# Kernel tuning notes

Measured on AMD Instinct MI355X. Metric: run time of the kernel, lower is better.

## Reference

```python
import jax, jax.numpy as jnp
import numpy as np

N = 50000          # num_nodes
E = 800000         # general (base) edge count
R_BASE = 3         # base relation types
R = 2 * R_BASE + 1 # base + inverse + self-loop relation
D_IN = 64
D_HID = 64
D_OUT = 64


def _glorot(k, shape):
    # xavier_uniform with relu gain, fan over last two dims
    gain = np.sqrt(2.0)
    bound = gain * np.sqrt(6.0 / (shape[-2] + shape[-1]))
    return jax.random.uniform(k, shape, jnp.float32, -bound, bound)


def setup_inputs() -> dict:
    key = jax.random.key(0)
    ks = jax.random.split(key, 6)
    x = jax.random.normal(ks[0], (N, D_IN), dtype=jnp.float32)
    src = jax.random.randint(ks[1], (E,), 0, N)
    dst = jax.random.randint(ks[2], (E,), 0, N)
    et = jax.random.randint(ks[3], (E,), 0, R_BASE)
    nodes = jnp.arange(N)
    # triples = [original edges, inverse edges (type+R_BASE), self-loops (type 2*R_BASE)]
    triples = jnp.concatenate([
        jnp.stack([src, et, dst], axis=1),
        jnp.stack([dst, et + R_BASE, src], axis=1),
        jnp.stack([nodes, jnp.full((N,), 2 * R_BASE), nodes], axis=1),
    ], axis=0).astype(jnp.int64)
    w1 = _glorot(ks[4], (R, D_IN, D_HID))
    w2 = _glorot(ks[5], (R, D_HID, D_OUT))
    b1 = jnp.zeros((D_HID,), jnp.float32)
    b2 = jnp.zeros((D_OUT,), jnp.float32)
    return {"x": x, "w1": w1, "b1": b1, "w2": w2, "b2": b2,
            "triples": triples, "num_nodes": N, "num_edge_types": R}


def _rgcn_layer(x, W, b, triples, num_nodes, num_rels):
    # vertical stacking: sparse adj [R*N, N], entry (r*N+src, dst) = 1, row-normalised
    src, et, dst = triples[:, 0], triples[:, 1], triples[:, 2]
    rows = et * num_nodes + src                     # [T] row index in stacked adj
    counts = jnp.zeros((num_rels * num_nodes,), x.dtype).at[rows].add(1.0)
    vals = 1.0 / counts[rows]                       # per-edge row-normalised weight
    msgs = vals[:, None] * x[dst]                   # [T, d] gathered + scaled messages
    af = jax.ops.segment_sum(msgs, rows, num_segments=num_rels * num_nodes)
    af = af.reshape(num_rels, num_nodes, x.shape[1])  # [R, N, d]
    return jnp.einsum('rio,rni->no', W, af) + b


def reference(x, w1, b1, w2, b2, triples, num_nodes, num_edge_types):
    h = _rgcn_layer(x, w1, b1, triples, num_nodes, num_edge_types)
    h = jax.nn.relu(h)
    out = _rgcn_layer(h, w2, b2, triples, num_nodes, num_edge_types)
    return out
```

## Files before the change

kernel.cpp:

```cpp
#include <hip/hip_runtime.h>
#include <stdint.h>

#define D 64
#define TILE 2048
#define PK 8
#define NBMAX 128
#define BW 512
#define RMAX 8

typedef __attribute__((ext_vector_type(8))) short bf16x8;
typedef __attribute__((ext_vector_type(4))) float f32x4;

__device__ __forceinline__ unsigned short f2bf(float f) {
    union { float f; unsigned int i; } v; v.f = f;
    unsigned int x = v.i;
    unsigned int r = (x + 0x7FFFu + ((x >> 16) & 1u)) >> 16;
    return (unsigned short)r;
}
__device__ __forceinline__ float lo_bf(unsigned int u) {
    union { unsigned int i; float f; } v; v.i = u << 16; return v.f;
}
__device__ __forceinline__ float hi_bf(unsigned int u) {
    union { unsigned int i; float f; } v; v.i = u & 0xFFFF0000u; return v.f;
}

__global__ void detect_kernel(const int* __restrict__ t32, int probe, int expect,
                              unsigned int* __restrict__ flag) {
    if (blockIdx.x == 0 && threadIdx.x == 0)
        flag[0] = (t32[probe] == expect) ? 0u : 1u;
}

__global__ void __launch_bounds__(256) binpass_kernel(const unsigned int* __restrict__ t32,
                                                      const unsigned int* __restrict__ flag,
                                                      unsigned int* __restrict__ staging,
                                                      unsigned int* __restrict__ binCnt,
                                                      int M, int NB, int CAP) {
    __shared__ unsigned int sorted[TILE];
    __shared__ unsigned char sortedb[TILE];
    __shared__ unsigned int hist[NBMAX];
    __shared__ unsigned int scan_[NBMAX];
    __shared__ unsigned int cur[NBMAX];
    __shared__ unsigned int gbase[NBMAX];

    int tid = threadIdx.x;
    int tileBase = blockIdx.x * TILE;

    for (int i = tid; i < NBMAX; i += 256) hist[i] = 0;
    __syncthreads();

    bool is64 = flag[0] != 0;
    unsigned int myE[PK];
    unsigned char myB[PK];
    #pragma unroll
    for (int k = 0; k < PK; k++) {
        int e = tileBase + tid * PK + k;
        myB[k] = 0xFF;
        if (e < M) {
            long w = (long)e * 3;
            unsigned int src, et, dst;
            if (is64) { src = t32[2*w]; et = t32[2*(w+1)]; dst = t32[2*(w+2)]; }
            else      { src = t32[w];   et = t32[w+1];     dst = t32[w+2]; }
            unsigned int b = src >> 9;
            unsigned int lsrc = src & (BW - 1);
            myE[k] = (lsrc << 20) | (et << 17) | dst;
            myB[k] = (unsigned char)b;
            atomicAdd(&hist[b], 1u);
        }
    }
    __syncthreads();

    if (tid < NBMAX) scan_[tid] = hist[tid];
    __syncthreads();
    for (int off = 1; off < NBMAX; off <<= 1) {
        unsigned int v = (tid < NBMAX && tid >= off) ? scan_[tid - off] : 0u;
        __syncthreads();
        if (tid < NBMAX) scan_[tid] += v;
        __syncthreads();
    }
    if (tid < NB) {
        gbase[tid] = atomicAdd(&binCnt[tid], hist[tid]);
        cur[tid] = scan_[tid] - hist[tid];
    }
    __syncthreads();

    #pragma unroll
    for (int k = 0; k < PK; k++) {
        if (myB[k] != 0xFF) {
            unsigned int p = atomicAdd(&cur[myB[k]], 1u);
            sorted[p] = myE[k];
            sortedb[p] = myB[k];
        }
    }
    __syncthreads();

    unsigned int total = scan_[NB - 1];
    for (unsigned int i = tid; i < total; i += 256) {
        unsigned int b = sortedb[i];
        unsigned int local = i - (scan_[b] - hist[b]);
        unsigned int slot = gbase[b] + local;
        if (slot < (unsigned int)CAP)
            staging[(size_t)b * CAP + slot] = sorted[i];
    }
}

__global__ void __launch_bounds__(512) buildcsr_kernel(const unsigned int* __restrict__ staging,
                                                       const unsigned int* __restrict__ binCnt,
                                                       unsigned int* __restrict__ segOff,
                                                       uint2* __restrict__ adj,
                                                       int M, int N, int R, int NB, int CAP) {
    __shared__ unsigned int hist7[RMAX * BW];
    __shared__ unsigned int curs7[RMAX * BW];
    __shared__ unsigned int scanbuf[BW];
    __shared__ unsigned int sbase[NBMAX];

    int b = blockIdx.x, tid = threadIdx.x;
    int nodeBase = b * BW;
    int nNodes = N - nodeBase; if (nNodes > BW) nNodes = BW;
    unsigned int cntB = binCnt[b]; if (cntB > (unsigned int)CAP) cntB = CAP;

    for (int i = tid; i < RMAX * BW; i += 512) hist7[i] = 0;
    __syncthreads();

    const unsigned int* st = staging + (size_t)b * CAP;
    for (unsigned int i = tid; i < cntB; i += 512) {
        unsigned int e = st[i];
        unsigned int lsrc = e >> 20, et = (e >> 17) & 7u;
        atomicAdd(&hist7[et * BW + lsrc], 1u);
    }
    __syncthreads();

    unsigned int d = 0;
    for (int r2 = 0; r2 < R; r2++) d += hist7[r2 * BW + tid];
    scanbuf[tid] = d;
    __syncthreads();
    for (int off = 1; off < BW; off <<= 1) {
        unsigned int v = (tid >= off) ? scanbuf[tid - off] : 0u;
        __syncthreads();
        scanbuf[tid] += v;
        __syncthreads();
    }

    if (tid < NBMAX) sbase[tid] = (tid < NB) ? min(binCnt[tid], (unsigned int)CAP) : 0u;
    __syncthreads();
    for (int off = 1; off < NBMAX; off <<= 1) {
        unsigned int v = (tid < NBMAX && tid >= off) ? sbase[tid - off] : 0u;
        __syncthreads();
        if (tid < NBMAX) sbase[tid] += v;
        __syncthreads();
    }
    unsigned int baseB = (b == 0) ? 0u : sbase[b - 1];

    unsigned int nodeStart = baseB + scanbuf[tid] - d;
    if (tid < nNodes) {
        unsigned int o = nodeStart;
        for (int et = 0; et < R; et++) {
            segOff[(size_t)(nodeBase + tid) * 8 + et] = o;
            curs7[et * BW + tid] = o;
            o += hist7[et * BW + tid];
        }
        segOff[(size_t)(nodeBase + tid) * 8 + R] = o;
    } else {
        for (int et = 0; et < R; et++) curs7[et * BW + tid] = 0;
    }
    __syncthreads();

    for (unsigned int i = tid; i < cntB; i += 512) {
        unsigned int e = st[i];
        unsigned int lsrc = e >> 20, et = (e >> 17) & 7u, dst = e & 0x1FFFFu;
        unsigned int pos = atomicAdd(&curs7[et * BW + lsrc], 1u);
        float val = 1.0f / (float)hist7[et * BW + lsrc];
        uint2 m; m.x = dst; m.y = __float_as_uint(val);
        adj[pos] = m;
    }
}

__global__ void convert_kernel(const float* __restrict__ x, unsigned short* __restrict__ xb, int total) {
    int i = (blockIdx.x * blockDim.x + threadIdx.x) * 4;
    if (i + 3 < total) {
        float4 v = *(const float4*)(x + i);
        ushort4 o; o.x = f2bf(v.x); o.y = f2bf(v.y); o.z = f2bf(v.z); o.w = f2bf(v.w);
        *(ushort4*)(xb + i) = o;
    } else {
        for (int j = i; j < total; j++) xb[j] = f2bf(x[j]);
    }
}

__global__ void packw_kernel(const float* __restrict__ W, unsigned short* __restrict__ wpack, int R) {
    int gid = blockIdx.x * blockDim.x + threadIdx.x;
    if (gid >= R * 512) return;
    int lane = gid & 63;
    int c = (gid >> 6) & 3;
    int t = (gid >> 8) & 1;
    int r = gid >> 9;
    int col = c * 16 + (lane & 15);
    int kbase = t * 32 + 8 * (lane >> 4);
    #pragma unroll
    for (int j = 0; j < 8; j++) {
        wpack[(size_t)gid * 8 + j] = f2bf(W[((size_t)r * D + kbase + j) * D + col]);
    }
}

template<int RM>
__global__ void __launch_bounds__(256) agg_kernel(const unsigned short* __restrict__ xtab,
                                                  const uint2* __restrict__ adj,
                                                  const unsigned int* __restrict__ segOff,
                                                  unsigned int* __restrict__ afcat,
                                                  int N, int totalWaves) {
    int w = blockIdx.x * 4 + (threadIdx.x >> 6);
    int lane = threadIdx.x & 63;
    int h = lane >> 4;
    int cq = lane & 15;
    const int stride = RM * 32;

    for (int n = w; n < N; n += totalWaves) {
        int nu = __builtin_amdgcn_readfirstlane(n);
        #pragma unroll
        for (int r = 0; r < RM; r++) {
            unsigned int s = segOff[(size_t)nu * 8 + r], e = segOff[(size_t)nu * 8 + r + 1];
            float a0 = 0.f, a1 = 0.f, a2 = 0.f, a3 = 0.f;
            unsigned int cnt = e - s;
            unsigned int iters = (cnt + 3) >> 2;
            #pragma unroll 2
            for (unsigned int it = 0; it < iters; ++it) {
                unsigned int idx = s + 4 * it + h;
                bool live = idx < e;
                uint2 m = adj[live ? idx : s];
                float val = live ? __uint_as_float(m.y) : 0.f;
                uint2 u = *(const uint2*)(xtab + (size_t)m.x * D + 4 * cq);
                a0 += val * lo_bf(u.x);
                a1 += val * hi_bf(u.x);
                a2 += val * lo_bf(u.y);
                a3 += val * hi_bf(u.y);
            }
            a0 += __shfl_xor(a0, 16); a1 += __shfl_xor(a1, 16);
            a2 += __shfl_xor(a2, 16); a3 += __shfl_xor(a3, 16);
            a0 += __shfl_xor(a0, 32); a1 += __shfl_xor(a1, 32);
            a2 += __shfl_xor(a2, 32); a3 += __shfl_xor(a3, 32);
            if (lane < 16) {
                uint2 o;
                o.x = ((unsigned int)f2bf(a1) << 16) | (unsigned int)f2bf(a0);
                o.y = ((unsigned int)f2bf(a3) << 16) | (unsigned int)f2bf(a2);
                *(uint2*)(afcat + (size_t)nu * stride + r * 32 + 2 * cq) = o;
            }
        }
    }
}

__global__ void __launch_bounds__(256) agg_kernel_dyn(const unsigned short* __restrict__ xtab,
                                                      const uint2* __restrict__ adj,
                                                      const unsigned int* __restrict__ segOff,
                                                      unsigned int* __restrict__ afcat,
                                                      int N, int totalWaves, int Rm1) {
    int w = blockIdx.x * 4 + (threadIdx.x >> 6);
    int lane = threadIdx.x & 63;
    int h = lane >> 4;
    int cq = lane & 15;
    int stride = Rm1 * 32;

    for (int n = w; n < N; n += totalWaves) {
        int nu = __builtin_amdgcn_readfirstlane(n);
        for (int r = 0; r < Rm1; r++) {
            unsigned int s = segOff[(size_t)nu * 8 + r], e = segOff[(size_t)nu * 8 + r + 1];
            float a0 = 0.f, a1 = 0.f, a2 = 0.f, a3 = 0.f;
            unsigned int cnt = e - s;
            unsigned int iters = (cnt + 3) >> 2;
            for (unsigned int it = 0; it < iters; ++it) {
                unsigned int idx = s + 4 * it + h;
                bool live = idx < e;
                uint2 m = adj[live ? idx : s];
                float val = live ? __uint_as_float(m.y) : 0.f;
                uint2 u = *(const uint2*)(xtab + (size_t)m.x * D + 4 * cq);
                a0 += val * lo_bf(u.x);
                a1 += val * hi_bf(u.x);
                a2 += val * lo_bf(u.y);
                a3 += val * hi_bf(u.y);
            }
            a0 += __shfl_xor(a0, 16); a1 += __shfl_xor(a1, 16);
            a2 += __shfl_xor(a2, 16); a3 += __shfl_xor(a3, 16);
            a0 += __shfl_xor(a0, 32); a1 += __shfl_xor(a1, 32);
            a2 += __shfl_xor(a2, 32); a3 += __shfl_xor(a3, 32);
            if (lane < 16) {
                uint2 o;
                o.x = ((unsigned int)f2bf(a1) << 16) | (unsigned int)f2bf(a0);
                o.y = ((unsigned int)f2bf(a3) << 16) | (unsigned int)f2bf(a2);
                *(uint2*)(afcat + (size_t)nu * stride + r * 32 + 2 * cq) = o;
            }
        }
    }
}

__global__ void __launch_bounds__(256) gemm2_kernel(const unsigned short* __restrict__ afcat,
                                                    const unsigned short* __restrict__ xtab,
                                                    const unsigned short* __restrict__ wpack,
                                                    const float* __restrict__ bias,
                                                    unsigned short* __restrict__ out_bf,
                                                    float* __restrict__ out_f32,
                                                    int N, int nchunks, int mode) {
    int wid = blockIdx.x * 4 + (threadIdx.x >> 6);
    int lane = threadIdx.x & 63;
    if (wid >= nchunks) return;
    int n0 = wid * 16;
    int arow = n0 + (lane & 15);
    if (arow >= N) arow = N - 1;
    int ksub = 8 * (lane >> 4);

    bf16x8 a[14];
    const unsigned short* af = afcat + (size_t)arow * 384 + ksub;
    #pragma unroll
    for (int kt = 0; kt < 12; kt++) a[kt] = *(const bf16x8*)(af + kt * 32);
    const unsigned short* xr = xtab + (size_t)arow * D + ksub;
    a[12] = *(const bf16x8*)(xr);
    a[13] = *(const bf16x8*)(xr + 32);

    const unsigned short* wp = wpack + (size_t)lane * 8;
    int colb = lane & 15;
    int rowbase = n0 + (lane >> 4) * 4;
    #pragma unroll
    for (int c = 0; c < 4; c++) {
        f32x4 acc = {0.f, 0.f, 0.f, 0.f};
        #pragma unroll
        for (int kt = 0; kt < 14; kt++) {
            bf16x8 bfr = *(const bf16x8*)(wp + (size_t)(kt * 4 + c) * 512);
            acc = __builtin_amdgcn_mfma_f32_16x16x32_bf16(a[kt], bfr, acc, 0, 0, 0);
        }
        int col = 16 * c + colb;
        float bl = bias[col];
        #pragma unroll
        for (int q = 0; q < 4; q++) {
            int row = rowbase + q;
            if (row < N) {
                float o = acc[q] + bl;
                if (mode == 0) out_bf[(size_t)row * D + col] = f2bf(fmaxf(o, 0.f));
                else           out_f32[(size_t)row * D + col] = o;
            }
        }
    }
}

extern "C" void kernel_launch(void* const* d_in, const int* in_sizes, int n_in,
                              void* d_out, int out_size, void* d_ws, size_t ws_size,
                              hipStream_t stream) {
    const float* x  = (const float*)d_in[0];
    const float* w1 = (const float*)d_in[1];
    const float* b1 = (const float*)d_in[2];
    const float* w2 = (const float*)d_in[3];
    const float* b2 = (const float*)d_in[4];
    const int* trip = (const int*)d_in[5];

    const int N = in_sizes[0] / D;
    const int R = in_sizes[1] / (D * D);
    const int M = in_sizes[5] / 3;

    const int NB = (N + BW - 1) / BW;
    const int CAP = (((2 * (M / NB)) + 1023) / 1024) * 1024;

    char* p = (char*)d_ws;
    auto alloc = [&](size_t bytes) { void* q = (void*)p; p += (bytes + 255) / 256 * 256; return q; };
    unsigned int* binCnt  = (unsigned int*)alloc((size_t)NBMAX * 4);
    unsigned int* segOff  = (unsigned int*)alloc((size_t)N * 8 * 4);
    unsigned int* flag    = (unsigned int*)alloc(256);
    unsigned int* staging = (unsigned int*)alloc((size_t)NB * CAP * 4);
    uint2*        adj     = (uint2*)alloc((size_t)M * 8);
    unsigned int* afcat   = (unsigned int*)alloc((size_t)N * (R - 1) * 32 * 4);
    unsigned short* xb    = (unsigned short*)alloc((size_t)N * D * 2);
    unsigned short* hb    = (unsigned short*)alloc((size_t)N * D * 2);
    unsigned short* wp1   = (unsigned short*)alloc((size_t)R * 512 * 8 * 2);
    unsigned short* wp2   = (unsigned short*)alloc((size_t)R * 512 * 8 * 2);

    hipMemsetAsync(binCnt, 0, (size_t)NBMAX * 4, stream);

    int probe = (M - N) * 3 + 1;
    detect_kernel<<<1, 1, 0, stream>>>(trip, probe, R - 1, flag);

    int tiles = (M + TILE - 1) / TILE;
    binpass_kernel<<<tiles, 256, 0, stream>>>((const unsigned int*)trip, flag, staging, binCnt, M, NB, CAP);
    buildcsr_kernel<<<NB, 512, 0, stream>>>(staging, binCnt, segOff, adj, M, N, R, NB, CAP);

    int totX = N * D;
    convert_kernel<<<(totX / 4 + 255) / 256, 256, 0, stream>>>(x, xb, totX);
    packw_kernel<<<(R * 512 + 255) / 256, 256, 0, stream>>>(w1, wp1, R);
    packw_kernel<<<(R * 512 + 255) / 256, 256, 0, stream>>>(w2, wp2, R);

    int gblocks = 2048, tw = gblocks * 4;
    int nchunks = (N + 15) / 16;
    int gemmb = (nchunks + 3) / 4;

    if (R - 1 == 6)
        agg_kernel<6><<<gblocks, 256, 0, stream>>>(xb, adj, segOff, afcat, N, tw);
    else
        agg_kernel_dyn<<<gblocks, 256, 0, stream>>>(xb, adj, segOff, afcat, N, tw, R - 1);
    gemm2_kernel<<<gemmb, 256, 0, stream>>>((const unsigned short*)afcat, xb, wp1, b1, hb, nullptr, N, nchunks, 0);

    if (R - 1 == 6)
        agg_kernel<6><<<gblocks, 256, 0, stream>>>(hb, adj, segOff, afcat, N, tw);
    else
        agg_kernel_dyn<<<gblocks, 256, 0, stream>>>(hb, adj, segOff, afcat, N, tw, R - 1);
    gemm2_kernel<<<gemmb, 256, 0, stream>>>((const unsigned short*)afcat, hb, wp2, b2, nullptr, (float*)d_out, N, nchunks, 1);
}
```

Baseline: 293.6 us.

## Map aggregation lanes to per-(node,relation) segments across node pairs

The aggregation kernels now process two nodes per wave, and each 16-lane group owns whole (node, relation) segments that it walks serially. Previously all four groups split the edges of one segment and then combined their partial sums with cross-lane shuffles. The goal is to remove the shuffle reductions and the predicated idle iterations on short segments. The cost is that groups can diverge on uneven segment lengths, and each group issues fewer parallel gathers per segment.

New measurement: 286.5 us. -2.4%, faster.

```diff
diff --git a/kernel.cpp b/kernel.cpp
--- a/kernel.cpp
+++ b/kernel.cpp
@@ -208,39 +208,41 @@
                                                   int N, int totalWaves) {
     int w = blockIdx.x * 4 + (threadIdx.x >> 6);
     int lane = threadIdx.x & 63;
-    int h = lane >> 4;
+    int g = lane >> 4;
     int cq = lane & 15;
     const int stride = RM * 32;
-
-    for (int n = w; n < N; n += totalWaves) {
-        int nu = __builtin_amdgcn_readfirstlane(n);
+    const int PERG = (2 * RM + 3) >> 2;
+    int npairs = (N + 1) >> 1;
+
+    for (int p = w; p < npairs; p += totalWaves) {
+        int n0 = 2 * p;
         #pragma unroll
-        for (int r = 0; r < RM; r++) {
-            unsigned int s = segOff[(size_t)nu * 8 + r], e = segOff[(size_t)nu * 8 + r + 1];
+        for (int k = 0; k < PERG; k++) {
+            int sidx = g * PERG + k;
+            int node = n0 + (sidx >= RM ? 1 : 0);
+            int r = sidx - (sidx >= RM ? RM : 0);
+            bool valid = node < N;
+            unsigned int s = 0, e = 0;
+            if (valid) {
+                s = segOff[(size_t)node * 8 + r];
+                e = segOff[(size_t)node * 8 + r + 1];
+            }
             float a0 = 0.f, a1 = 0.f, a2 = 0.f, a3 = 0.f;
-            unsigned int cnt = e - s;
-            unsigned int iters = (cnt + 3) >> 2;
             #pragma unroll 2
-            for (unsigned int it = 0; it < iters; ++it) {
-                unsigned int idx = s + 4 * it + h;
-                bool live = idx < e;
-                uint2 m = adj[live ? idx : s];
-                float val = live ? __uint_as_float(m.y) : 0.f;
+            for (unsigned int idx = s; idx < e; ++idx) {
+                uint2 m = adj[idx];
+                float val = __uint_as_float(m.y);
                 uint2 u = *(const uint2*)(xtab + (size_t)m.x * D + 4 * cq);
                 a0 += val * lo_bf(u.x);
                 a1 += val * hi_bf(u.x);
                 a2 += val * lo_bf(u.y);
                 a3 += val * hi_bf(u.y);
             }
-            a0 += __shfl_xor(a0, 16); a1 += __shfl_xor(a1, 16);
-            a2 += __shfl_xor(a2, 16); a3 += __shfl_xor(a3, 16);
-            a0 += __shfl_xor(a0, 32); a1 += __shfl_xor(a1, 32);
-            a2 += __shfl_xor(a2, 32); a3 += __shfl_xor(a3, 32);
-            if (lane < 16) {
+            if (valid) {
                 uint2 o;
                 o.x = ((unsigned int)f2bf(a1) << 16) | (unsigned int)f2bf(a0);
                 o.y = ((unsigned int)f2bf(a3) << 16) | (unsigned int)f2bf(a2);
-                *(uint2*)(afcat + (size_t)nu * stride + r * 32 + 2 * cq) = o;
+                *(uint2*)(afcat + (size_t)node * stride + r * 32 + 2 * cq) = o;
             }
         }
     }
@@ -253,37 +255,39 @@
                                                       int N, int totalWaves, int Rm1) {
     int w = blockIdx.x * 4 + (threadIdx.x >> 6);
     int lane = threadIdx.x & 63;
-    int h = lane >> 4;
+    int g = lane >> 4;
     int cq = lane & 15;
     int stride = Rm1 * 32;
-
-    for (int n = w; n < N; n += totalWaves) {
-        int nu = __builtin_amdgcn_readfirstlane(n);
-        for (int r = 0; r < Rm1; r++) {
-            unsigned int s = segOff[(size_t)nu * 8 + r], e = segOff[(size_t)nu * 8 + r + 1];
+    int PERG = (2 * Rm1 + 3) >> 2;
+    int npairs = (N + 1) >> 1;
+
+    for (int p = w; p < npairs; p += totalWaves) {
+        int n0 = 2 * p;
+        for (int k = 0; k < PERG; k++) {
+            int sidx = g * PERG + k;
+            int node = n0 + (sidx >= Rm1 ? 1 : 0);
+            int r = sidx - (sidx >= Rm1 ? Rm1 : 0);
+            bool valid = (node < N) && (sidx < 2 * Rm1);
+            unsigned int s = 0, e = 0;
+            if (valid) {
+                s = segOff[(size_t)node * 8 + r];
+                e = segOff[(size_t)node * 8 + r + 1];
+            }
             float a0 = 0.f, a1 = 0.f, a2 = 0.f, a3 = 0.f;
-            unsigned int cnt = e - s;
-            unsigned int iters = (cnt + 3) >> 2;
-            for (unsigned int it = 0; it < iters; ++it) {
-                unsigned int idx = s + 4 * it + h;
-                bool live = idx < e;
-                uint2 m = adj[live ? idx : s];
-                float val = live ? __uint_as_float(m.y) : 0.f;
+            for (unsigned int idx = s; idx < e; ++idx) {
+                uint2 m = adj[idx];
+                float val = __uint_as_float(m.y);
                 uint2 u = *(const uint2*)(xtab + (size_t)m.x * D + 4 * cq);
                 a0 += val * lo_bf(u.x);
                 a1 += val * hi_bf(u.x);
                 a2 += val * lo_bf(u.y);
                 a3 += val * hi_bf(u.y);
             }
-            a0 += __shfl_xor(a0, 16); a1 += __shfl_xor(a1, 16);
-            a2 += __shfl_xor(a2, 16); a3 += __shfl_xor(a3, 16);
-            a0 += __shfl_xor(a0, 32); a1 += __shfl_xor(a1, 32);
-            a2 += __shfl_xor(a2, 32); a3 += __shfl_xor(a3, 32);
-            if (lane < 16) {
+            if (valid) {
                 uint2 o;
                 o.x = ((unsigned int)f2bf(a1) << 16) | (unsigned int)f2bf(a0);
                 o.y = ((unsigned int)f2bf(a3) << 16) | (unsigned int)f2bf(a2);
-                *(uint2*)(afcat + (size_t)nu * stride + r * 32 + 2 * cq) = o;
+                *(uint2*)(afcat + (size_t)node * stride + r * 32 + 2 * cq) = o;
             }
         }
     }
```
